# Kernel optimization log

Hardware: AMD Instinct MI355X
Metric: run time of the kernel (lower is better)

Reference implementation:

```python
import jax, jax.numpy as jnp
import numpy as np

N = 50000          # nodes
E = 1_000_000      # edges
NODE_DIM = 16
EMB = 64           # embed_dim
OUT = 64           # out_dim per head
EA_DIM = 8         # raw edge_attr_dim
HEADS = 8
SLOPE = 0.01       # leaky_relu default negative slope
LN_EPS = 1e-5


def mlp(x, w, b, g, beta):
    # MLP(in, out): Linear -> LayerNorm -> ReLU (standard block in this repo)
    y = x @ w + b
    mu = jnp.mean(y, axis=-1, keepdims=True)
    var = jnp.var(y, axis=-1, keepdims=True)
    y = (y - mu) / jnp.sqrt(var + LN_EPS) * g + beta
    return jax.nn.relu(y)


def gat_layer(x, ea, src, tgt, W, a):
    """AA_GATlayer forward (dropout = identity at eval).
    x: [N, in], ea: [E, EMB], W: [in, OUT], a: [2*OUT + EMB]."""
    h = x @ W                                  # [N, OUT]
    d = h.shape[1]
    a_src, a_tgt, a_edge = a[:d], a[d:2 * d], a[2 * d:]
    # score = leaky_relu(a @ concat([h_src, h_tgt, ea])) without materializing the concat
    s = jax.nn.leaky_relu(h[src] @ a_src + h[tgt] @ a_tgt + ea @ a_edge, SLOPE)  # [E]
    s = s - jnp.max(s)
    e = jnp.exp(s)
    denom = jax.ops.segment_sum(e, src, num_segments=N)          # [N]
    attn = e / (denom[src] + 1e-16)                              # [E]
    h_prime = jax.ops.segment_sum(h[tgt] * attn[:, None], src, num_segments=N)  # [N, OUT]
    return jax.nn.elu(h_prime)


def setup_inputs() -> dict:
    key = jax.random.key(0)
    ks = jax.random.split(key, 16)
    sc = lambda fan_in: 1.0 / np.sqrt(fan_in)
    inp = {}
    inp["X"] = jax.random.normal(ks[0], (N, NODE_DIM), jnp.float32)
    inp["edge_attr"] = jax.random.normal(ks[1], (E, EA_DIM), jnp.float32)
    inp["edge_index"] = jax.random.randint(ks[2], (2, E), 0, N, jnp.int64)
    inp["matched_car_infra_nodes"] = jax.random.randint(ks[3], (1000,), 0, N, jnp.int64)
    # node_embed MLP params
    inp["w_node"] = jax.random.uniform(ks[4], (NODE_DIM, EMB), jnp.float32, -sc(NODE_DIM), sc(NODE_DIM))
    inp["b_node"] = jnp.zeros((EMB,), jnp.float32)
    inp["g_node"] = jnp.ones((EMB,), jnp.float32)
    inp["beta_node"] = jnp.zeros((EMB,), jnp.float32)
    # edge_attr_embed MLP params
    inp["w_edge"] = jax.random.uniform(ks[5], (EA_DIM, EMB), jnp.float32, -sc(EA_DIM), sc(EA_DIM))
    inp["b_edge"] = jnp.zeros((EMB,), jnp.float32)
    inp["g_edge"] = jnp.ones((EMB,), jnp.float32)
    inp["beta_edge"] = jnp.zeros((EMB,), jnp.float32)
    # 8 GAT heads: W [EMB,OUT], a [2*OUT+EMB]
    inp["gat_W"] = jax.random.uniform(ks[6], (HEADS, EMB, OUT), jnp.float32, -sc(EMB), sc(EMB))
    inp["gat_a"] = jax.random.uniform(ks[7], (HEADS, 2 * OUT + EMB), jnp.float32, -sc(2 * OUT + EMB), sc(2 * OUT + EMB))
    # output GAT layer: W [OUT*HEADS, OUT], a [2*OUT+EMB]
    inp["out_W"] = jax.random.uniform(ks[8], (OUT * HEADS, OUT), jnp.float32, -sc(OUT * HEADS), sc(OUT * HEADS))
    inp["out_a"] = jax.random.uniform(ks[9], (2 * OUT + EMB,), jnp.float32, -sc(2 * OUT + EMB), sc(2 * OUT + EMB))
    return inp


def reference(X, edge_attr, w_node, b_node, g_node, beta_node,
              w_edge, b_edge, g_edge, beta_edge,
              gat_W, gat_a, out_W, out_a,
              edge_index, matched_car_infra_nodes):
    src, tgt = edge_index[0], edge_index[1]
    x = mlp(X, w_node, b_node, g_node, beta_node)                  # [N, EMB]
    ea = mlp(edge_attr, w_edge, b_edge, g_edge, beta_edge)         # [E, EMB]
    heads = [gat_layer(x, ea, src, tgt, gat_W[i], gat_a[i]) for i in range(HEADS)]
    xh = jax.nn.elu(jnp.concatenate(heads, axis=1))                # [N, OUT*HEADS]
    out = gat_layer(xh, ea, src, tgt, out_W, out_a)                # [N, OUT]
    return jax.nn.log_softmax(out, axis=1)
```

## Files before the change

### kernel.cpp

```cpp
#include <hip/hip_runtime.h>
#include <hip/hip_fp16.h>

#define NN 50000
#define EE 1000000
#define HALF 25000

typedef _Float16 h8v __attribute__((ext_vector_type(8)));
typedef float    f4a __attribute__((ext_vector_type(4)));

__device__ __forceinline__ float wsum(float v){
#pragma unroll
  for(int m=1;m<64;m<<=1) v += __shfl_xor(v,m,64);
  return v;
}
__device__ __forceinline__ unsigned encf(float f){
  unsigned u = __float_as_uint(f);
  return (u & 0x80000000u) ? ~u : (u | 0x80000000u);
}
__device__ __forceinline__ float decf(unsigned u){
  u = (u & 0x80000000u) ? (u & 0x7fffffffu) : ~u;
  return __uint_as_float(u);
}

__global__ __launch_bounds__(256) void zero_k(int* counts, int* cursor, unsigned* mx){
  int i = blockIdx.x*blockDim.x + threadIdx.x;
  if(i < NN){ counts[i] = 0; cursor[i] = 0; }
  if(i < 64) mx[i] = 0u;
}

__global__ __launch_bounds__(64) void cvec_k(const float* __restrict__ gat_W, const float* __restrict__ gat_a,
                                             float* __restrict__ cdir){
  int h = blockIdx.x, k = threadIdx.x;
  const float* W = gat_W + (size_t)h*64*64;
  const float* a = gat_a + (size_t)h*192;
  float cs = 0.f, ct = 0.f;
#pragma unroll
  for(int j=0;j<64;j++){ float wv = W[k*64+j]; cs += wv*a[j]; ct += wv*a[64+j]; }
  cdir[h*64 + k]       = cs;
  cdir[512 + h*64 + k] = ct;
}

__global__ __launch_bounds__(256) void cvtw_k(const float* __restrict__ gat_W, const float* __restrict__ out_W,
                                              __half* __restrict__ WT, __half* __restrict__ OT){
  int h = blockIdx.x; int tid = threadIdx.x;
  for(int idx = tid; idx < 4096; idx += 256){
    int j = idx >> 6, k = idx & 63;
    WT[(size_t)h*4096 + k*64 + j] = __float2half(gat_W[(size_t)h*4096 + j*64 + k]);
    OT[(size_t)h*4096 + k*64 + j] = __float2half(out_W[(size_t)h*4096 + j*64 + k]);
  }
}

__global__ __launch_bounds__(256) void node_mlp(const float* __restrict__ X, const float* __restrict__ w,
                                                const float* __restrict__ b, const float* __restrict__ g,
                                                const float* __restrict__ beta, const float* __restrict__ cdir,
                                                __half* __restrict__ x, float* __restrict__ ps8,
                                                float* __restrict__ pt8){
  int wid  = (blockIdx.x*blockDim.x + threadIdx.x) >> 6;
  int lane = threadIdx.x & 63;
  if(wid >= NN) return;
  float acc = b[lane];
#pragma unroll
  for(int k=0;k<16;k++) acc += X[wid*16+k] * w[k*64+lane];
  float mu  = wsum(acc) * (1.0f/64.0f);
  float d   = acc - mu;
  float var = wsum(d*d) * (1.0f/64.0f);
  float y   = d * rsqrtf(var + 1e-5f) * g[lane] + beta[lane];
  float xv  = fmaxf(y, 0.0f);
  x[(size_t)wid*64 + lane] = __float2half(xv);
#pragma unroll 1
  for(int h=0;h<8;h++){
    float a = wsum(xv * cdir[h*64+lane]);
    float c = wsum(xv * cdir[512 + h*64+lane]);
    if(lane == 0){ ps8[wid*8+h] = a; pt8[wid*8+h] = c; }
  }
}

__global__ __launch_bounds__(256) void hist_k(const int* __restrict__ src, int* __restrict__ counts){
  int e = blockIdx.x*blockDim.x + threadIdx.x;
  if(e < EE){
    int s = src[e];
    if((unsigned)s >= NN) s = 0;
    atomicAdd(&counts[s], 1);
  }
}

__global__ __launch_bounds__(256) void scan1_k(const int* __restrict__ counts, int* __restrict__ bsum){
  int i = blockIdx.x*256 + threadIdx.x;
  int v = (i < NN) ? counts[i] : 0;
  int s = v;
#pragma unroll
  for(int m=1;m<64;m<<=1) s += __shfl_xor(s,m,64);
  __shared__ int sm[4];
  if((threadIdx.x & 63) == 0) sm[threadIdx.x>>6] = s;
  __syncthreads();
  if(threadIdx.x == 0) bsum[blockIdx.x] = sm[0]+sm[1]+sm[2]+sm[3];
}

__global__ __launch_bounds__(256) void scan2_k(const int* __restrict__ bsum, int* __restrict__ bpre,
                                               int* __restrict__ offs){
  const int NB = (NN + 255)/256;
  int t = threadIdx.x;
  __shared__ int sm[256];
  int v = (t < NB) ? bsum[t] : 0;
  sm[t] = v; __syncthreads();
  for(int off=1; off<256; off<<=1){
    int u = (t >= off) ? sm[t-off] : 0;
    __syncthreads();
    sm[t] += u;
    __syncthreads();
  }
  if(t < NB) bpre[t] = sm[t] - v;
  if(t == 0) offs[NN] = EE;
}

__global__ __launch_bounds__(256) void scan3_k(const int* __restrict__ counts, const int* __restrict__ bpre,
                                               int* __restrict__ offs){
  int i = blockIdx.x*256 + threadIdx.x;
  int t = threadIdx.x;
  __shared__ int sm[256];
  int v = (i < NN) ? counts[i] : 0;
  sm[t] = v; __syncthreads();
  for(int off=1; off<256; off<<=1){
    int u = (t >= off) ? sm[t-off] : 0;
    __syncthreads();
    sm[t] += u;
    __syncthreads();
  }
  if(i < NN) offs[i] = bpre[blockIdx.x] + sm[t] - v;
}

__global__ __launch_bounds__(256) void scatter_k(const int* __restrict__ src, const int* __restrict__ tgt,
                                                 const int* __restrict__ offs, int* __restrict__ cursor,
                                                 int* __restrict__ rank, int* __restrict__ tgt_s,
                                                 int* __restrict__ src_s){
  int e = blockIdx.x*blockDim.x + threadIdx.x;
  if(e < EE){
    int s = src[e];
    if((unsigned)s >= NN) s = 0;
    int pos = offs[s] + atomicAdd(&cursor[s], 1);
    rank[e] = pos;
    int t = tgt[e];
    if((unsigned)t >= NN) t = 0;
    tgt_s[pos] = t;
    src_s[pos] = s;
  }
}

__global__ __launch_bounds__(256) void edge_mlp_q(const int* __restrict__ rank, const float* __restrict__ ea,
                                                  const float* __restrict__ w, const float* __restrict__ b,
                                                  const float* __restrict__ g, const float* __restrict__ beta,
                                                  const float* __restrict__ gat_a, const float* __restrict__ out_a,
                                                  float* __restrict__ q8, float* __restrict__ q_out){
  __shared__ float wle[512];
  __shared__ float ble[64], gle[64], bbe[64];
  __shared__ float ale[64*12];
  int tid = threadIdx.x;
  for(int idx=tid; idx<512; idx+=256){ int j=idx>>3, k=idx&7; wle[idx] = w[k*64+j]; }
  if(tid < 64){
    ble[tid] = b[tid]; gle[tid] = g[tid]; bbe[tid] = beta[tid];
#pragma unroll
    for(int r=0;r<8;r++) ale[tid*12+r] = gat_a[r*192 + 128 + tid];
    ale[tid*12+8] = out_a[128 + tid];
  }
  __syncthreads();
  int e = blockIdx.x*blockDim.x + tid;
  if(e >= EE) return;
  float4 ia = ((const float4*)ea)[(size_t)e*2];
  float4 ib = ((const float4*)ea)[(size_t)e*2+1];
  float y[64];
#pragma unroll
  for(int j=0;j<64;j++){
    float4 w0 = *(const float4*)&wle[j*8];
    float4 w1 = *(const float4*)&wle[j*8+4];
    float acc = ble[j];
    acc = fmaf(ia.x,w0.x, fmaf(ia.y,w0.y, fmaf(ia.z,w0.z, fmaf(ia.w,w0.w, acc))));
    acc = fmaf(ib.x,w1.x, fmaf(ib.y,w1.y, fmaf(ib.z,w1.z, fmaf(ib.w,w1.w, acc))));
    y[j] = acc;
  }
  float mu = 0.f;
#pragma unroll
  for(int j=0;j<64;j++) mu += y[j];
  mu *= (1.0f/64.0f);
  float var = 0.f;
#pragma unroll
  for(int j=0;j<64;j++){ float d = y[j]-mu; var += d*d; }
  var *= (1.0f/64.0f);
  float inv = rsqrtf(var + 1e-5f);
#pragma unroll
  for(int j=0;j<64;j++) y[j] = fmaxf((y[j]-mu)*inv*gle[j] + bbe[j], 0.0f);
  float qv[9];
#pragma unroll
  for(int r=0;r<9;r++) qv[r] = 0.f;
#pragma unroll
  for(int j=0;j<64;j++){
    float4 a0 = *(const float4*)&ale[j*12];
    float4 a1 = *(const float4*)&ale[j*12+4];
    float a8  = ale[j*12+8];
    float yj = y[j];
    qv[0]=fmaf(yj,a0.x,qv[0]); qv[1]=fmaf(yj,a0.y,qv[1]); qv[2]=fmaf(yj,a0.z,qv[2]); qv[3]=fmaf(yj,a0.w,qv[3]);
    qv[4]=fmaf(yj,a1.x,qv[4]); qv[5]=fmaf(yj,a1.y,qv[5]); qv[6]=fmaf(yj,a1.z,qv[6]); qv[7]=fmaf(yj,a1.w,qv[7]);
    qv[8]=fmaf(yj,a8 ,qv[8]);
  }
  int r = rank[e];
  ((float4*)q8)[(size_t)r*2]   = make_float4(qv[0],qv[1],qv[2],qv[3]);
  ((float4*)q8)[(size_t)r*2+1] = make_float4(qv[4],qv[5],qv[6],qv[7]);
  q_out[r] = qv[8];
}

__global__ __launch_bounds__(256) void maxq_k(const float* __restrict__ q8, const float* __restrict__ q_out,
                                              unsigned* __restrict__ mx){
  float m[9];
#pragma unroll
  for(int r=0;r<9;r++) m[r] = -3.0e38f;
  for(int i = blockIdx.x*256 + threadIdx.x; i < EE; i += gridDim.x*256){
    float4 a = ((const float4*)q8)[(size_t)i*2];
    float4 c = ((const float4*)q8)[(size_t)i*2+1];
    m[0]=fmaxf(m[0],a.x); m[1]=fmaxf(m[1],a.y); m[2]=fmaxf(m[2],a.z); m[3]=fmaxf(m[3],a.w);
    m[4]=fmaxf(m[4],c.x); m[5]=fmaxf(m[5],c.y); m[6]=fmaxf(m[6],c.z); m[7]=fmaxf(m[7],c.w);
    m[8]=fmaxf(m[8], q_out[i]);
  }
#pragma unroll
  for(int r=0;r<9;r++)
#pragma unroll
    for(int msk=1;msk<64;msk<<=1) m[r] = fmaxf(m[r], __shfl_xor(m[r],msk,64));
  __shared__ float sm[4][9];
  int wv = threadIdx.x>>6, lane = threadIdx.x&63;
  if(lane == 0){
#pragma unroll
    for(int r=0;r<9;r++) sm[wv][r] = m[r];
  }
  __syncthreads();
  if(threadIdx.x < 9){
    int r = threadIdx.x;
    float v = fmaxf(fmaxf(sm[0][r],sm[1][r]), fmaxf(sm[2][r],sm[3][r]));
    atomicMax(&mx[r], encf(v));
  }
}

__global__ __launch_bounds__(256) void maxp_k(const float* __restrict__ ps8, const float* __restrict__ pt8,
                                              unsigned* __restrict__ mx){
  float m[16];
#pragma unroll
  for(int r=0;r<16;r++) m[r] = -3.0e38f;
  for(int i = blockIdx.x*256 + threadIdx.x; i < NN; i += gridDim.x*256){
    float4 a = ((const float4*)ps8)[(size_t)i*2];
    float4 c = ((const float4*)ps8)[(size_t)i*2+1];
    float4 d = ((const float4*)pt8)[(size_t)i*2];
    float4 e = ((const float4*)pt8)[(size_t)i*2+1];
    m[0]=fmaxf(m[0],a.x); m[1]=fmaxf(m[1],a.y); m[2]=fmaxf(m[2],a.z); m[3]=fmaxf(m[3],a.w);
    m[4]=fmaxf(m[4],c.x); m[5]=fmaxf(m[5],c.y); m[6]=fmaxf(m[6],c.z); m[7]=fmaxf(m[7],c.w);
    m[8]=fmaxf(m[8],d.x); m[9]=fmaxf(m[9],d.y); m[10]=fmaxf(m[10],d.z); m[11]=fmaxf(m[11],d.w);
    m[12]=fmaxf(m[12],e.x); m[13]=fmaxf(m[13],e.y); m[14]=fmaxf(m[14],e.z); m[15]=fmaxf(m[15],e.w);
  }
#pragma unroll
  for(int r=0;r<16;r++)
#pragma unroll
    for(int msk=1;msk<64;msk<<=1) m[r] = fmaxf(m[r], __shfl_xor(m[r],msk,64));
  __shared__ float sm[4][16];
  int wv = threadIdx.x>>6, lane = threadIdx.x&63;
  if(lane == 0){
#pragma unroll
    for(int r=0;r<16;r++) sm[wv][r] = m[r];
  }
  __syncthreads();
  if(threadIdx.x < 16){
    int r = threadIdx.x;
    float v = fmaxf(fmaxf(sm[0][r],sm[1][r]), fmaxf(sm[2][r],sm[3][r]));
    atomicMax(&mx[16+r], encf(v));
  }
}

__global__ __launch_bounds__(256) void maxpo_k(const float* __restrict__ ps_o, const float* __restrict__ pt_o,
                                               unsigned* __restrict__ mx){
  float m0 = -3.0e38f, m1 = -3.0e38f;
  for(int i = blockIdx.x*256 + threadIdx.x; i < NN; i += gridDim.x*256){
    m0 = fmaxf(m0, ps_o[i]); m1 = fmaxf(m1, pt_o[i]);
  }
#pragma unroll
  for(int msk=1;msk<64;msk<<=1){ m0=fmaxf(m0,__shfl_xor(m0,msk,64)); m1=fmaxf(m1,__shfl_xor(m1,msk,64)); }
  __shared__ float sm[4][2];
  int wv = threadIdx.x>>6, lane = threadIdx.x&63;
  if(lane == 0){ sm[wv][0]=m0; sm[wv][1]=m1; }
  __syncthreads();
  if(threadIdx.x < 2){
    int r = threadIdx.x;
    float v = fmaxf(fmaxf(sm[0][r],sm[1][r]), fmaxf(sm[2][r],sm[3][r]));
    atomicMax(&mx[32+r], encf(v));
  }
}

__global__ __launch_bounds__(256) void score_k(const int* __restrict__ src_s, const int* __restrict__ tgt_s,
                                               const float* __restrict__ ps8, const float* __restrict__ pt8,
                                               const unsigned* __restrict__ mx, const float* __restrict__ q8,
                                               __half* __restrict__ w8h){
  int i = blockIdx.x*256 + threadIdx.x;
  if(i >= EE) return;
  int s = src_s[i], t = tgt_s[i];
  float4 qa = ((const float4*)q8)[(size_t)i*2];
  float4 qb = ((const float4*)q8)[(size_t)i*2+1];
  float4 sa = ((const float4*)ps8)[(size_t)s*2];
  float4 sb = ((const float4*)ps8)[(size_t)s*2+1];
  float4 ta = ((const float4*)pt8)[(size_t)t*2];
  float4 tb = ((const float4*)pt8)[(size_t)t*2+1];
  float sv[8] = {qa.x+sa.x+ta.x, qa.y+sa.y+ta.y, qa.z+sa.z+ta.z, qa.w+sa.w+ta.w,
                 qb.x+sb.x+tb.x, qb.y+sb.y+tb.y, qb.z+sb.z+tb.z, qb.w+sb.w+tb.w};
  float wv[8];
#pragma unroll
  for(int h=0;h<8;h++){
    float B = decf(mx[h]) + decf(mx[16+h]) + decf(mx[24+h]);
    float M = (B > 0.f) ? B : 0.01f*B;
    float x = sv[h];
    x = (x > 0.f) ? x : 0.01f*x;
    wv[h] = __expf(x - M);
  }
  __half2 p01 = __floats2half2_rn(wv[0],wv[1]);
  __half2 p23 = __floats2half2_rn(wv[2],wv[3]);
  __half2 p45 = __floats2half2_rn(wv[4],wv[5]);
  __half2 p67 = __floats2half2_rn(wv[6],wv[7]);
  uint4 pk;
  pk.x = *(unsigned*)&p01; pk.y = *(unsigned*)&p23;
  pk.z = *(unsigned*)&p45; pk.w = *(unsigned*)&p67;
  *(uint4*)(w8h + (size_t)i*8) = pk;
}

__global__ __launch_bounds__(256) void score_out_k(const int* __restrict__ src_s, const int* __restrict__ tgt_s,
                                                   const float* __restrict__ ps_o, const float* __restrict__ pt_o,
                                                   const unsigned* __restrict__ mx, float* __restrict__ q_out){
  int i = blockIdx.x*256 + threadIdx.x;
  if(i >= EE) return;
  float B = decf(mx[8]) + decf(mx[32]) + decf(mx[33]);
  float M = (B > 0.f) ? B : 0.01f*B;
  float x = ps_o[src_s[i]] + pt_o[tgt_s[i]] + q_out[i];
  x = (x > 0.f) ? x : 0.01f*x;
  q_out[i] = __expf(x - M);
}

__global__ __launch_bounds__(256) void agg_k(const int* __restrict__ offs, const int* __restrict__ tgt_s,
    const __half* __restrict__ w8h, const __half* __restrict__ x, __half* __restrict__ pre, int nbase){
  int wid  = nbase + ((blockIdx.x*blockDim.x + threadIdx.x) >> 6);
  int lane = threadIdx.x & 63;
  int quad = lane >> 4, l16 = lane & 15;
  int b  = offs[wid];
  int e2 = offs[wid+1];
  float  den[8];
  float4 num[8];
#pragma unroll
  for(int h=0;h<8;h++){ den[h] = 0.f; num[h] = make_float4(0.f,0.f,0.f,0.f); }
  for(int i=b+quad; i<e2; i+=4){
    int t = tgt_s[i];
    uint4 rw = *(const uint4*)(w8h + (size_t)i*8);
    float2 w01 = __half22float2(*(const __half2*)&rw.x);
    float2 w23 = __half22float2(*(const __half2*)&rw.y);
    float2 w45 = __half22float2(*(const __half2*)&rw.z);
    float2 w67 = __half22float2(*(const __half2*)&rw.w);
    uint2 raw = *(const uint2*)(x + (size_t)t*64 + l16*4);
    float2 fa = __half22float2(*(const __half2*)&raw.x);
    float2 fb = __half22float2(*(const __half2*)&raw.y);
    float4 xv = make_float4(fa.x, fa.y, fb.x, fb.y);
    float wv[8] = {w01.x,w01.y,w23.x,w23.y, w45.x,w45.y,w67.x,w67.y};
#pragma unroll
    for(int h=0;h<8;h++){
      den[h]   += wv[h];
      num[h].x = fmaf(wv[h],xv.x,num[h].x); num[h].y = fmaf(wv[h],xv.y,num[h].y);
      num[h].z = fmaf(wv[h],xv.z,num[h].z); num[h].w = fmaf(wv[h],xv.w,num[h].w);
    }
  }
#pragma unroll
  for(int h=0;h<8;h++){
    den[h]   += __shfl_xor(den[h],16,64);   den[h]   += __shfl_xor(den[h],32,64);
    num[h].x += __shfl_xor(num[h].x,16,64); num[h].x += __shfl_xor(num[h].x,32,64);
    num[h].y += __shfl_xor(num[h].y,16,64); num[h].y += __shfl_xor(num[h].y,32,64);
    num[h].z += __shfl_xor(num[h].z,16,64); num[h].z += __shfl_xor(num[h].z,32,64);
    num[h].w += __shfl_xor(num[h].w,16,64); num[h].w += __shfl_xor(num[h].w,32,64);
  }
  __half* dst = pre + (size_t)(wid - nbase)*512;
#pragma unroll
  for(int k=0;k<2;k++){
    int h = 2*quad + k;
    float invd = (den[h] > 0.f) ? 1.0f/den[h] : 0.f;
    __half2 h0 = __floats2half2_rn(num[h].x*invd, num[h].y*invd);
    __half2 h1 = __floats2half2_rn(num[h].z*invd, num[h].w*invd);
    uint2 pk; pk.x = *(unsigned*)&h0; pk.y = *(unsigned*)&h1;
    *(uint2*)(dst + h*64 + l16*4) = pk;
  }
}

__global__ __launch_bounds__(256) void transform_mfma(const __half* __restrict__ pre,
                                                      const __half* __restrict__ WT,
                                                      const __half* __restrict__ OT,
                                                      float* __restrict__ h2p,
                                                      int nbase, int cn){
  __shared__ __half zl[4*16*64];
  int tid = threadIdx.x;
  int w  = tid >> 6, l = tid & 63;
  int lr = l & 15, lg = l >> 4;
  int n0 = blockIdx.x * 64;
  int g  = blockIdx.y;
  h2p += (size_t)g * NN * 64;
  int gn  = n0 + w*16 + lr;
  int gnr = (gn < cn) ? gn : 0;
  __half* zw = zl + w*1024;
  f4a out[4];
#pragma unroll
  for(int i=0;i<4;i++){ out[i][0]=0.f; out[i][1]=0.f; out[i][2]=0.f; out[i][3]=0.f; }
#pragma unroll 1
  for(int hh=0; hh<4; hh++){
    int h = g*4 + hh;
    h8v a1_0 = *(const h8v*)(pre + (size_t)gnr*512 + h*64 + 0*32 + lg*8);
    h8v a1_1 = *(const h8v*)(pre + (size_t)gnr*512 + h*64 + 1*32 + lg*8);
    f4a zacc[4];
#pragma unroll
    for(int nt=0; nt<4; nt++){ zacc[nt][0]=0.f; zacc[nt][1]=0.f; zacc[nt][2]=0.f; zacc[nt][3]=0.f; }
    const __half* WTh = WT + (size_t)h*4096;
#pragma unroll
    for(int nt=0; nt<4; nt++){
      h8v b0 = *(const h8v*)(WTh + (nt*16 + lr)*64 + 0*32 + lg*8);
      h8v b1 = *(const h8v*)(WTh + (nt*16 + lr)*64 + 1*32 + lg*8);
      zacc[nt] = __builtin_amdgcn_mfma_f32_16x16x32_f16(a1_0, b0, zacc[nt], 0, 0, 0);
      zacc[nt] = __builtin_amdgcn_mfma_f32_16x16x32_f16(a1_1, b1, zacc[nt], 0, 0, 0);
    }
#pragma unroll
    for(int nt=0; nt<4; nt++){
#pragma unroll
      for(int r=0; r<4; r++){
        float v = zacc[nt][r];
        float z = (v > 0.f) ? v : expm1f(v);
        z = (z > 0.f) ? z : expm1f(z);
        int rho = lg*4 + r;
        int c   = nt*16 + lr;
        int pc  = (((c>>3) ^ (rho&7))<<3) | (c&7);
        zw[rho*64 + pc] = __float2half(z);
      }
    }
    const __half* OTh = OT + (size_t)h*4096;
#pragma unroll
    for(int ks=0; ks<2; ks++){
      int Gp = (lg + 4*ks) ^ (lr & 7);
      h8v a2 = *(const h8v*)(zw + lr*64 + Gp*8);
#pragma unroll
      for(int nt=0; nt<4; nt++){
        h8v b2 = *(const h8v*)(OTh + (nt*16 + lr)*64 + ks*32 + lg*8);
        out[nt] = __builtin_amdgcn_mfma_f32_16x16x32_f16(a2, b2, out[nt], 0, 0, 0);
      }
    }
  }
#pragma unroll
  for(int nt=0; nt<4; nt++){
#pragma unroll
    for(int r=0; r<4; r++){
      int grow = n0 + w*16 + lg*4 + r;
      if(grow < cn) h2p[(size_t)(nbase + grow)*64 + nt*16 + lr] = out[nt][r];
    }
  }
}

__global__ __launch_bounds__(256) void finalize_po(const float* __restrict__ p0, const float* __restrict__ p1,
                                                   const float* __restrict__ out_a, __half* __restrict__ h2f,
                                                   float* __restrict__ ps_o, float* __restrict__ pt_o){
  int wid  = (blockIdx.x*blockDim.x + threadIdx.x) >> 6;
  int lane = threadIdx.x & 63;
  if(wid >= NN) return;
  float v = p0[(size_t)wid*64 + lane] + p1[(size_t)wid*64 + lane];
  float ps = wsum(v * out_a[lane]);
  float pt = wsum(v * out_a[64+lane]);
  if(lane == 0){ ps_o[wid] = ps; pt_o[wid] = pt; }
  h2f[(size_t)wid*64 + lane] = __float2half(v);
}

__global__ __launch_bounds__(256) void agg_out(const int* __restrict__ offs, const int* __restrict__ tgt_s,
                                               const float* __restrict__ w_out, const __half* __restrict__ h2f,
                                               float* __restrict__ dout){
  int wid  = (blockIdx.x*blockDim.x + threadIdx.x) >> 6;
  int lane = threadIdx.x & 63;
  if(wid >= NN) return;
  int quad = lane >> 4, l16 = lane & 15;
  int b  = offs[wid];
  int e2 = offs[wid+1];
  float4 num = make_float4(0.f,0.f,0.f,0.f);
  float den = 0.f;
  for(int i=b+quad; i<e2; i+=4){
    int t = tgt_s[i];
    float w = w_out[i];
    uint2 raw = *(const uint2*)(h2f + (size_t)t*64 + l16*4);
    float2 fa = __half22float2(*(const __half2*)&raw.x);
    float2 fb = __half22float2(*(const __half2*)&raw.y);
    den += w;
    num.x = fmaf(w,fa.x,num.x); num.y = fmaf(w,fa.y,num.y);
    num.z = fmaf(w,fb.x,num.z); num.w = fmaf(w,fb.y,num.w);
  }
  den   += __shfl_xor(den,16,64);   den   += __shfl_xor(den,32,64);
  num.x += __shfl_xor(num.x,16,64); num.x += __shfl_xor(num.x,32,64);
  num.y += __shfl_xor(num.y,16,64); num.y += __shfl_xor(num.y,32,64);
  num.z += __shfl_xor(num.z,16,64); num.z += __shfl_xor(num.z,32,64);
  num.w += __shfl_xor(num.w,16,64); num.w += __shfl_xor(num.w,32,64);
  float inv = (den > 0.f) ? 1.0f/den : 0.f;
  float z[4];
  float mloc = -3.0e38f;
#pragma unroll
  for(int k=0;k<4;k++){
    float hp = ((&num.x)[k]) * inv;
    z[k] = (hp > 0.f) ? hp : expm1f(hp);
    mloc = fmaxf(mloc, z[k]);
  }
#pragma unroll
  for(int msk=1; msk<16; msk<<=1) mloc = fmaxf(mloc, __shfl_xor(mloc,msk,64));
  float ssum = 0.f;
#pragma unroll
  for(int k=0;k<4;k++) ssum += __expf(z[k] - mloc);
#pragma unroll
  for(int msk=1; msk<16; msk<<=1) ssum += __shfl_xor(ssum,msk,64);
  float lse = mloc + logf(ssum);
  if(quad == 0){
    float4 o = make_float4(z[0]-lse, z[1]-lse, z[2]-lse, z[3]-lse);
    ((float4*)dout)[(size_t)wid*16 + l16] = o;
  }
}

extern "C" void kernel_launch(void* const* d_in, const int* in_sizes, int n_in,
                              void* d_out, int out_size, void* d_ws, size_t ws_size,
                              hipStream_t stream) {
  const float* X         = (const float*)d_in[0];
  const float* edge_attr = (const float*)d_in[1];
  const int*   edge_index= (const int*)d_in[2];
  const float* w_node    = (const float*)d_in[4];
  const float* b_node    = (const float*)d_in[5];
  const float* g_node    = (const float*)d_in[6];
  const float* beta_node = (const float*)d_in[7];
  const float* w_edge    = (const float*)d_in[8];
  const float* b_edge    = (const float*)d_in[9];
  const float* g_edge    = (const float*)d_in[10];
  const float* beta_edge = (const float*)d_in[11];
  const float* gat_W     = (const float*)d_in[12];
  const float* gat_a     = (const float*)d_in[13];
  const float* out_W     = (const float*)d_in[14];
  const float* out_a     = (const float*)d_in[15];
  float* dout = (float*)d_out;

  const int* src = edge_index;
  const int* tgt = edge_index + EE;

  char* base = (char*)d_ws;
  size_t off = 0;
  auto take = [&](size_t bytes)->char*{ char* p = base + off; off += (bytes + 31) & ~(size_t)31; return p; };
  int*      counts = (int*)     take((size_t)NN*4);
  int*      cursor = (int*)     take((size_t)NN*4);
  int*      offs   = (int*)     take((size_t)(NN+1)*4);
  int*      bsum   = (int*)     take(256*4);
  int*      bpre   = (int*)     take(256*4);
  unsigned* mx     = (unsigned*)take(64*4);
  float*    ps_o   = (float*)   take((size_t)NN*4);
  float*    pt_o   = (float*)   take((size_t)NN*4);
  float*    cdir   = (float*)   take(1024*4);
  int*      rank   = (int*)     take((size_t)EE*4);
  int*      tgt_s  = (int*)     take((size_t)EE*4);
  int*      src_s  = (int*)     take((size_t)EE*4);
  float*    ps8    = (float*)   take((size_t)NN*8*4);
  float*    pt8    = (float*)   take((size_t)NN*8*4);
  __half*   xh     = (__half*)  take((size_t)NN*64*2);
  __half*   h2fh   = (__half*)  take((size_t)NN*64*2);
  __half*   WT16   = (__half*)  take((size_t)8*4096*2);
  __half*   OT16   = (__half*)  take((size_t)8*4096*2);
  float*    h2p    = (float*)   take((size_t)2*NN*64*4);
  float*    q8     = (float*)   take((size_t)EE*8*4);
  __half*   w8h    = (__half*)  take((size_t)EE*8*2);
  float*    q_out  = (float*)   take((size_t)EE*4);
  __half*   pre    = (__half*)  take((size_t)HALF*512*2);

  const int NBLK_N  = (NN*64 + 255)/256;
  const int NBLK_E  = (EE + 255)/256;
  const int NBLK_S  = (NN + 255)/256;
  const int NBLK_A  = HALF/4;
  const int NBLK_T  = (HALF + 63)/64;

  zero_k   <<<NBLK_S, 256, 0, stream>>>(counts, cursor, mx);
  cvec_k   <<<8,       64, 0, stream>>>(gat_W, gat_a, cdir);
  cvtw_k   <<<8,      256, 0, stream>>>(gat_W, out_W, WT16, OT16);
  node_mlp <<<NBLK_N, 256, 0, stream>>>(X, w_node, b_node, g_node, beta_node, cdir, xh, ps8, pt8);
  hist_k   <<<NBLK_E, 256, 0, stream>>>(src, counts);
  scan1_k  <<<NBLK_S, 256, 0, stream>>>(counts, bsum);
  scan2_k  <<<1,      256, 0, stream>>>(bsum, bpre, offs);
  scan3_k  <<<NBLK_S, 256, 0, stream>>>(counts, bpre, offs);
  scatter_k<<<NBLK_E, 256, 0, stream>>>(src, tgt, offs, cursor, rank, tgt_s, src_s);
  edge_mlp_q<<<NBLK_E,256, 0, stream>>>(rank, edge_attr, w_edge, b_edge, g_edge, beta_edge,
                                        gat_a, out_a, q8, q_out);
  maxq_k   <<<1024,   256, 0, stream>>>(q8, q_out, mx);
  maxp_k   <<<128,    256, 0, stream>>>(ps8, pt8, mx);
  score_k  <<<NBLK_E, 256, 0, stream>>>(src_s, tgt_s, ps8, pt8, mx, q8, w8h);

  for(int half=0; half<2; half++){
    int nbase = half*HALF;
    agg_k<<<NBLK_A, 256, 0, stream>>>(offs, tgt_s, w8h, xh, pre, nbase);
    dim3 tg((unsigned)NBLK_T, 2);
    transform_mfma<<<tg, 256, 0, stream>>>(pre, WT16, OT16, h2p, nbase, HALF);
  }

  finalize_po<<<NBLK_N, 256, 0, stream>>>(h2p, h2p + (size_t)NN*64, out_a, h2fh, ps_o, pt_o);
  maxpo_k    <<<128,  256, 0, stream>>>(ps_o, pt_o, mx);
  score_out_k<<<NBLK_E,256, 0, stream>>>(src_s, tgt_s, ps_o, pt_o, mx, q_out);
  agg_out    <<<NBLK_N,256, 0, stream>>>(offs, tgt_s, q_out, h2fh, dout);
}
```

Baseline: 685.9 us.

## Fuse edge-score max into edge MLP and output scoring into aggregation

```diff
diff --git a/kernel.cpp b/kernel.cpp
--- a/kernel.cpp
+++ b/kernel.cpp
@@ -7,6 +7,8 @@
 
 typedef _Float16 h8v __attribute__((ext_vector_type(8)));
 typedef float    f4a __attribute__((ext_vector_type(4)));
+typedef unsigned u2v __attribute__((ext_vector_type(2)));
+typedef float    f4v __attribute__((ext_vector_type(4)));
 
 __device__ __forceinline__ float wsum(float v){
 #pragma unroll
@@ -150,10 +152,12 @@
                                                   const float* __restrict__ w, const float* __restrict__ b,
                                                   const float* __restrict__ g, const float* __restrict__ beta,
                                                   const float* __restrict__ gat_a, const float* __restrict__ out_a,
-                                                  float* __restrict__ q8, float* __restrict__ q_out){
+                                                  float* __restrict__ q8, float* __restrict__ q_out,
+                                                  unsigned* __restrict__ mx){
   __shared__ float wle[512];
   __shared__ float ble[64], gle[64], bbe[64];
   __shared__ float ale[64*12];
+  __shared__ float smx[4][9];
   int tid = threadIdx.x;
   for(int idx=tid; idx<512; idx+=256){ int j=idx>>3, k=idx&7; wle[idx] = w[k*64+j]; }
   if(tid < 64){
@@ -164,76 +168,64 @@
   }
   __syncthreads();
   int e = blockIdx.x*blockDim.x + tid;
-  if(e >= EE) return;
-  float4 ia = ((const float4*)ea)[(size_t)e*2];
-  float4 ib = ((const float4*)ea)[(size_t)e*2+1];
-  float y[64];
-#pragma unroll
-  for(int j=0;j<64;j++){
-    float4 w0 = *(const float4*)&wle[j*8];
-    float4 w1 = *(const float4*)&wle[j*8+4];
-    float acc = ble[j];
-    acc = fmaf(ia.x,w0.x, fmaf(ia.y,w0.y, fmaf(ia.z,w0.z, fmaf(ia.w,w0.w, acc))));
-    acc = fmaf(ib.x,w1.x, fmaf(ib.y,w1.y, fmaf(ib.z,w1.z, fmaf(ib.w,w1.w, acc))));
-    y[j] = acc;
-  }
-  float mu = 0.f;
-#pragma unroll
-  for(int j=0;j<64;j++) mu += y[j];
-  mu *= (1.0f/64.0f);
-  float var = 0.f;
-#pragma unroll
-  for(int j=0;j<64;j++){ float d = y[j]-mu; var += d*d; }
-  var *= (1.0f/64.0f);
-  float inv = rsqrtf(var + 1e-5f);
-#pragma unroll
-  for(int j=0;j<64;j++) y[j] = fmaxf((y[j]-mu)*inv*gle[j] + bbe[j], 0.0f);
   float qv[9];
-#pragma unroll
-  for(int r=0;r<9;r++) qv[r] = 0.f;
-#pragma unroll
-  for(int j=0;j<64;j++){
-    float4 a0 = *(const float4*)&ale[j*12];
-    float4 a1 = *(const float4*)&ale[j*12+4];
-    float a8  = ale[j*12+8];
-    float yj = y[j];
-    qv[0]=fmaf(yj,a0.x,qv[0]); qv[1]=fmaf(yj,a0.y,qv[1]); qv[2]=fmaf(yj,a0.z,qv[2]); qv[3]=fmaf(yj,a0.w,qv[3]);
-    qv[4]=fmaf(yj,a1.x,qv[4]); qv[5]=fmaf(yj,a1.y,qv[5]); qv[6]=fmaf(yj,a1.z,qv[6]); qv[7]=fmaf(yj,a1.w,qv[7]);
-    qv[8]=fmaf(yj,a8 ,qv[8]);
-  }
-  int r = rank[e];
-  ((float4*)q8)[(size_t)r*2]   = make_float4(qv[0],qv[1],qv[2],qv[3]);
-  ((float4*)q8)[(size_t)r*2+1] = make_float4(qv[4],qv[5],qv[6],qv[7]);
-  q_out[r] = qv[8];
-}
-
-__global__ __launch_bounds__(256) void maxq_k(const float* __restrict__ q8, const float* __restrict__ q_out,
-                                              unsigned* __restrict__ mx){
-  float m[9];
-#pragma unroll
-  for(int r=0;r<9;r++) m[r] = -3.0e38f;
-  for(int i = blockIdx.x*256 + threadIdx.x; i < EE; i += gridDim.x*256){
-    float4 a = ((const float4*)q8)[(size_t)i*2];
-    float4 c = ((const float4*)q8)[(size_t)i*2+1];
-    m[0]=fmaxf(m[0],a.x); m[1]=fmaxf(m[1],a.y); m[2]=fmaxf(m[2],a.z); m[3]=fmaxf(m[3],a.w);
-    m[4]=fmaxf(m[4],c.x); m[5]=fmaxf(m[5],c.y); m[6]=fmaxf(m[6],c.z); m[7]=fmaxf(m[7],c.w);
-    m[8]=fmaxf(m[8], q_out[i]);
+  if(e < EE){
+    float4 ia = ((const float4*)ea)[(size_t)e*2];
+    float4 ib = ((const float4*)ea)[(size_t)e*2+1];
+    float y[64];
+#pragma unroll
+    for(int j=0;j<64;j++){
+      float4 w0 = *(const float4*)&wle[j*8];
+      float4 w1 = *(const float4*)&wle[j*8+4];
+      float acc = ble[j];
+      acc = fmaf(ia.x,w0.x, fmaf(ia.y,w0.y, fmaf(ia.z,w0.z, fmaf(ia.w,w0.w, acc))));
+      acc = fmaf(ib.x,w1.x, fmaf(ib.y,w1.y, fmaf(ib.z,w1.z, fmaf(ib.w,w1.w, acc))));
+      y[j] = acc;
+    }
+    float mu = 0.f;
+#pragma unroll
+    for(int j=0;j<64;j++) mu += y[j];
+    mu *= (1.0f/64.0f);
+    float var = 0.f;
+#pragma unroll
+    for(int j=0;j<64;j++){ float d = y[j]-mu; var += d*d; }
+    var *= (1.0f/64.0f);
+    float inv = rsqrtf(var + 1e-5f);
+#pragma unroll
+    for(int j=0;j<64;j++) y[j] = fmaxf((y[j]-mu)*inv*gle[j] + bbe[j], 0.0f);
+#pragma unroll
+    for(int r=0;r<9;r++) qv[r] = 0.f;
+#pragma unroll
+    for(int j=0;j<64;j++){
+      float4 a0 = *(const float4*)&ale[j*12];
+      float4 a1 = *(const float4*)&ale[j*12+4];
+      float a8  = ale[j*12+8];
+      float yj = y[j];
+      qv[0]=fmaf(yj,a0.x,qv[0]); qv[1]=fmaf(yj,a0.y,qv[1]); qv[2]=fmaf(yj,a0.z,qv[2]); qv[3]=fmaf(yj,a0.w,qv[3]);
+      qv[4]=fmaf(yj,a1.x,qv[4]); qv[5]=fmaf(yj,a1.y,qv[5]); qv[6]=fmaf(yj,a1.z,qv[6]); qv[7]=fmaf(yj,a1.w,qv[7]);
+      qv[8]=fmaf(yj,a8 ,qv[8]);
+    }
+    int r = rank[e];
+    ((float4*)q8)[(size_t)r*2]   = make_float4(qv[0],qv[1],qv[2],qv[3]);
+    ((float4*)q8)[(size_t)r*2+1] = make_float4(qv[4],qv[5],qv[6],qv[7]);
+    q_out[r] = qv[8];
+  } else {
+#pragma unroll
+    for(int r=0;r<9;r++) qv[r] = -3.0e38f;
   }
 #pragma unroll
   for(int r=0;r<9;r++)
 #pragma unroll
-    for(int msk=1;msk<64;msk<<=1) m[r] = fmaxf(m[r], __shfl_xor(m[r],msk,64));
-  __shared__ float sm[4][9];
-  int wv = threadIdx.x>>6, lane = threadIdx.x&63;
+    for(int m=1;m<64;m<<=1) qv[r] = fmaxf(qv[r], __shfl_xor(qv[r],m,64));
+  int wv = tid>>6, lane = tid&63;
   if(lane == 0){
 #pragma unroll
-    for(int r=0;r<9;r++) sm[wv][r] = m[r];
+    for(int r=0;r<9;r++) smx[wv][r] = qv[r];
   }
   __syncthreads();
-  if(threadIdx.x < 9){
-    int r = threadIdx.x;
-    float v = fmaxf(fmaxf(sm[0][r],sm[1][r]), fmaxf(sm[2][r],sm[3][r]));
-    atomicMax(&mx[r], encf(v));
+  if(tid < 9){
+    float v = fmaxf(fmaxf(smx[0][tid],smx[1][tid]), fmaxf(smx[2][tid],smx[3][tid]));
+    atomicMax(&mx[tid], encf(v));
   }
 }
 
@@ -323,18 +315,6 @@
   *(uint4*)(w8h + (size_t)i*8) = pk;
 }
 
-__global__ __launch_bounds__(256) void score_out_k(const int* __restrict__ src_s, const int* __restrict__ tgt_s,
-                                                   const float* __restrict__ ps_o, const float* __restrict__ pt_o,
-                                                   const unsigned* __restrict__ mx, float* __restrict__ q_out){
-  int i = blockIdx.x*256 + threadIdx.x;
-  if(i >= EE) return;
-  float B = decf(mx[8]) + decf(mx[32]) + decf(mx[33]);
-  float M = (B > 0.f) ? B : 0.01f*B;
-  float x = ps_o[src_s[i]] + pt_o[tgt_s[i]] + q_out[i];
-  x = (x > 0.f) ? x : 0.01f*x;
-  q_out[i] = __expf(x - M);
-}
-
 __global__ __launch_bounds__(256) void agg_k(const int* __restrict__ offs, const int* __restrict__ tgt_s,
     const __half* __restrict__ w8h, const __half* __restrict__ x, __half* __restrict__ pre, int nbase){
   int wid  = nbase + ((blockIdx.x*blockDim.x + threadIdx.x) >> 6);
@@ -380,8 +360,8 @@
     float invd = (den[h] > 0.f) ? 1.0f/den[h] : 0.f;
     __half2 h0 = __floats2half2_rn(num[h].x*invd, num[h].y*invd);
     __half2 h1 = __floats2half2_rn(num[h].z*invd, num[h].w*invd);
-    uint2 pk; pk.x = *(unsigned*)&h0; pk.y = *(unsigned*)&h1;
-    *(uint2*)(dst + h*64 + l16*4) = pk;
+    u2v pk; pk.x = *(unsigned*)&h0; pk.y = *(unsigned*)&h1;
+    __builtin_nontemporal_store(pk, (u2v*)(dst + h*64 + l16*4));
   }
 }
 
@@ -449,7 +429,7 @@
 #pragma unroll
     for(int r=0; r<4; r++){
       int grow = n0 + w*16 + lg*4 + r;
-      if(grow < cn) h2p[(size_t)(nbase + grow)*64 + nt*16 + lr] = out[nt][r];
+      if(grow < cn) __builtin_nontemporal_store(out[nt][r], &h2p[(size_t)(nbase + grow)*64 + nt*16 + lr]);
     }
   }
 }
@@ -468,19 +448,25 @@
 }
 
 __global__ __launch_bounds__(256) void agg_out(const int* __restrict__ offs, const int* __restrict__ tgt_s,
-                                               const float* __restrict__ w_out, const __half* __restrict__ h2f,
-                                               float* __restrict__ dout){
+                                               const float* __restrict__ q_out, const float* __restrict__ ps_o,
+                                               const float* __restrict__ pt_o, const unsigned* __restrict__ mx,
+                                               const __half* __restrict__ h2f, float* __restrict__ dout){
   int wid  = (blockIdx.x*blockDim.x + threadIdx.x) >> 6;
   int lane = threadIdx.x & 63;
   if(wid >= NN) return;
   int quad = lane >> 4, l16 = lane & 15;
   int b  = offs[wid];
   int e2 = offs[wid+1];
+  float B = decf(mx[8]) + decf(mx[32]) + decf(mx[33]);
+  float M = (B > 0.f) ? B : 0.01f*B;
+  float pso = ps_o[wid];
   float4 num = make_float4(0.f,0.f,0.f,0.f);
   float den = 0.f;
   for(int i=b+quad; i<e2; i+=4){
     int t = tgt_s[i];
-    float w = w_out[i];
+    float sv = q_out[i] + pso + pt_o[t];
+    sv = (sv > 0.f) ? sv : 0.01f*sv;
+    float w = __expf(sv - M);
     uint2 raw = *(const uint2*)(h2f + (size_t)t*64 + l16*4);
     float2 fa = __half22float2(*(const __half2*)&raw.x);
     float2 fb = __half22float2(*(const __half2*)&raw.y);
@@ -511,8 +497,8 @@
   for(int msk=1; msk<16; msk<<=1) ssum += __shfl_xor(ssum,msk,64);
   float lse = mloc + logf(ssum);
   if(quad == 0){
-    float4 o = make_float4(z[0]-lse, z[1]-lse, z[2]-lse, z[3]-lse);
-    ((float4*)dout)[(size_t)wid*16 + l16] = o;
+    f4v o; o.x = z[0]-lse; o.y = z[1]-lse; o.z = z[2]-lse; o.w = z[3]-lse;
+    __builtin_nontemporal_store(o, (f4v*)(dout + (size_t)wid*64 + l16*4));
   }
 }
 
@@ -582,8 +568,7 @@
   scan3_k  <<<NBLK_S, 256, 0, stream>>>(counts, bpre, offs);
   scatter_k<<<NBLK_E, 256, 0, stream>>>(src, tgt, offs, cursor, rank, tgt_s, src_s);
   edge_mlp_q<<<NBLK_E,256, 0, stream>>>(rank, edge_attr, w_edge, b_edge, g_edge, beta_edge,
-                                        gat_a, out_a, q8, q_out);
-  maxq_k   <<<1024,   256, 0, stream>>>(q8, q_out, mx);
+                                        gat_a, out_a, q8, q_out, mx);
   maxp_k   <<<128,    256, 0, stream>>>(ps8, pt8, mx);
   score_k  <<<NBLK_E, 256, 0, stream>>>(src_s, tgt_s, ps8, pt8, mx, q8, w8h);
 
@@ -596,6 +581,5 @@
 
   finalize_po<<<NBLK_N, 256, 0, stream>>>(h2p, h2p + (size_t)NN*64, out_a, h2fh, ps_o, pt_o);
   maxpo_k    <<<128,  256, 0, stream>>>(ps_o, pt_o, mx);
-  score_out_k<<<NBLK_E,256, 0, stream>>>(src_s, tgt_s, ps_o, pt_o, mx, q_out);
-  agg_out    <<<NBLK_N,256, 0, stream>>>(offs, tgt_s, q_out, h2fh, dout);
-}
+  agg_out    <<<NBLK_N,256, 0, stream>>>(offs, tgt_s, q_out, ps_o, pt_o, mx, h2fh, dout);
+}
```

Result: no change. 684.3 us (-0.2%).
